# Kernel tuning notes

Hardware: AMD Instinct MI355X
Metric: run time of the kernel (lower is better)

## Reference

```python
import jax, jax.numpy as jnp
import numpy as np

B, L, C, H, NL = 128, 1024, 256, 256, 2


def setup_inputs() -> dict:
    key = jax.random.key(0)
    ks = jax.random.split(key, 10)
    s = 1.0 / np.sqrt(H)  # PyTorch GRUCell init scale
    return {
        "x": jax.random.normal(ks[0], (B, L, C), dtype=jnp.float32),
        "h0": jnp.zeros((NL, B, H), dtype=jnp.float32),
        "w_ih0": jax.random.normal(ks[1], (3 * H, C), dtype=jnp.float32) * s,
        "w_hh0": jax.random.normal(ks[2], (3 * H, H), dtype=jnp.float32) * s,
        "b_ih0": jax.random.normal(ks[3], (3 * H,), dtype=jnp.float32) * s,
        "b_hh0": jax.random.normal(ks[4], (3 * H,), dtype=jnp.float32) * s,
        "w_ih1": jax.random.normal(ks[5], (3 * H, H), dtype=jnp.float32) * s,
        "w_hh1": jax.random.normal(ks[6], (3 * H, H), dtype=jnp.float32) * s,
        "b_ih1": jax.random.normal(ks[7], (3 * H,), dtype=jnp.float32) * s,
        "b_hh1": jax.random.normal(ks[8], (3 * H,), dtype=jnp.float32) * s,
    }


def gru_cell(x, h, w_ih, w_hh, b_ih, b_hh):
    # PyTorch GRUCell math
    gi = x @ w_ih.T + b_ih          # [B, 3H]
    gh = h @ w_hh.T + b_hh          # [B, 3H]
    i_r, i_z, i_n = jnp.split(gi, 3, axis=-1)
    h_r, h_z, h_n = jnp.split(gh, 3, axis=-1)
    r = jax.nn.sigmoid(i_r + h_r)
    z = jax.nn.sigmoid(i_z + h_z)
    n = jnp.tanh(i_n + r * h_n)
    return (1.0 - z) * n + z * h


def reference(x, h0, w_ih0, w_hh0, b_ih0, b_hh0, w_ih1, w_hh1, b_ih1, b_hh1):
    # Dropout layers act as identity in eval mode (faithful deterministic reference).
    def step(carry, xt):
        h_0, h_1 = carry
        h_0 = gru_cell(xt, h_0, w_ih0, w_hh0, b_ih0, b_hh0)
        h_1 = gru_cell(h_0, h_1, w_ih1, w_hh1, b_ih1, b_hh1)
        return (h_0, h_1), h_1

    xs = jnp.swapaxes(x, 0, 1)  # [L, B, C]
    (hf0, hf1), ys = jax.lax.scan(step, (h0[0], h0[1]), xs)
    out = jnp.swapaxes(ys, 0, 1)  # [B, L, H]
    return out, jnp.stack([hf0, hf1], axis=0)
```

## Files before the change

kernel.cpp:

```cpp
#include <hip/hip_runtime.h>
#include <stdint.h>

#define Bsz 128
#define Lsz 1024
#define Hsz 256
#define HB  (Bsz * Hsz)

typedef __attribute__((ext_vector_type(8))) short bf16x8;
typedef __attribute__((ext_vector_type(4))) float f32x4;

__device__ __forceinline__ unsigned short f2bf(float f) {
    union { float f; uint32_t u; } v; v.f = f;
    uint32_t u = v.u;
    return (unsigned short)((u + 0x7FFFu + ((u >> 16) & 1u)) >> 16);
}

__device__ __forceinline__ bf16x8 load_wfrag(const float* __restrict__ W, int row, int kb) {
    const float4* p = (const float4*)(W + row * Hsz + kb);
    float4 a = p[0], b = p[1];
    bf16x8 r;
    r[0] = (short)f2bf(a.x); r[1] = (short)f2bf(a.y);
    r[2] = (short)f2bf(a.z); r[3] = (short)f2bf(a.w);
    r[4] = (short)f2bf(b.x); r[5] = (short)f2bf(b.y);
    r[6] = (short)f2bf(b.z); r[7] = (short)f2bf(b.w);
    return r;
}

__device__ __forceinline__ float sigm(float x) { return 1.0f / (1.0f + __expf(-x)); }
__device__ __forceinline__ float tanhf_(float x) { return 1.0f - 2.0f / (1.0f + __expf(2.0f * x)); }

__device__ __forceinline__ void mm_step(bf16x8 a, const bf16x8 (&W)[3][8], int kt,
                                        f32x4& r, f32x4& z, f32x4& n) {
    r = __builtin_amdgcn_mfma_f32_16x16x32_bf16(a, W[0][kt], r, 0, 0, 0);
    z = __builtin_amdgcn_mfma_f32_16x16x32_bf16(a, W[1][kt], z, 0, 0, 0);
    n = __builtin_amdgcn_mfma_f32_16x16x32_bf16(a, W[2][kt], n, 0, 0, 0);
}


__device__ __forceinline__ bf16x8 ld_h_sc1(const unsigned short* p) {
    bf16x8 r;
    asm volatile("global_load_dwordx4 %0, %1, off sc1" : "=v"(r) : "v"(p));
    return r;
}

__device__ __forceinline__ void st_h_sc1(unsigned short* p, unsigned short v) {
    unsigned int d = v;
    asm volatile("global_store_short %0, %1, off sc1" :: "v"(p), "v"(d) : "memory");
}

__device__ __forceinline__ void drain_stores_then_flag8(int* flg_base, int entry, int val, int ln) {
    asm volatile("s_waitcnt vmcnt(0)" ::: "memory");
    if (ln < 8)
        __hip_atomic_store(flg_base + (ln << 5) + entry, val,
                           __ATOMIC_RELAXED, __HIP_MEMORY_SCOPE_AGENT);
}

__device__ __forceinline__ void waitflags16(const int* f, int target, int ln) {
    const int idx = ln & 15;
    while (__hip_atomic_load(f + idx, __ATOMIC_RELAXED, __HIP_MEMORY_SCOPE_AGENT) < target) {
        __builtin_amdgcn_s_sleep(1);
    }
    asm volatile("" ::: "memory");
}

__global__ void init_ws(const float* __restrict__ h0in, int* flags,
                        unsigned short* h0buf, unsigned short* h1buf) {
    int i = blockIdx.x * blockDim.x + threadIdx.x;
    if (i < 4096)
        __hip_atomic_store(flags + i, 0, __ATOMIC_RELAXED, __HIP_MEMORY_SCOPE_AGENT);
    st_h_sc1(&h0buf[HB + i], f2bf(h0in[i]));
    st_h_sc1(&h1buf[HB + i], f2bf(h0in[HB + i]));
    asm volatile("s_waitcnt vmcnt(0)" ::: "memory");
}

__global__ __launch_bounds__(512, 2) void gru2_persist(
    const float* __restrict__ x, const float* __restrict__ h0in,
    const float* __restrict__ wih0, const float* __restrict__ whh0,
    const float* __restrict__ bih0, const float* __restrict__ bhh0,
    const float* __restrict__ wih1, const float* __restrict__ whh1,
    const float* __restrict__ bih1, const float* __restrict__ bhh1,
    float* __restrict__ out,
    int* flags0, unsigned short* h0buf, unsigned short* h1buf)
{
    __shared__ float lds0[3][2][16][16];
    __shared__ float lds1[3][2][16][16];

    const int tid = threadIdx.x;
    const int wv = tid >> 6, ln = tid & 63;
    const int lr = ln & 15, quad = ln >> 4;
    const int g = blockIdx.x & 7, p = blockIdx.x >> 3;
    const int mat = wv & 3, jt = wv >> 2;
    const int b0 = g << 4;
    const int jabs = (p << 5) + (jt << 4) + lr;

    int* fl0g = flags0 + (g << 8);
    int* fl1g = flags0 + 2048 + (g << 8);
    int* myf0 = fl0g + (p << 5);
    int* myf1 = fl1g + (p << 5);

    const float* Wm = (mat == 0) ? wih0 : (mat == 1) ? whh0 : (mat == 2) ? wih1 : whh1;
    bf16x8 Wf[3][8];
#pragma unroll
    for (int gg = 0; gg < 3; ++gg)
#pragma unroll
        for (int kt = 0; kt < 8; ++kt)
            Wf[gg][kt] = load_wfrag(Wm, gg * Hsz + jabs, (kt << 5) + (quad << 3));

    float hp[4] = {0.f, 0.f, 0.f, 0.f};
    float bsr = 0.f, bsz_ = 0.f, bin_ = 0.f, bhn_ = 0.f;
    if (mat == 1) {
#pragma unroll
        for (int q = 0; q < 4; ++q) hp[q] = h0in[(b0 + (quad << 2) + q) * Hsz + jabs];
        bsr = bih0[jabs] + bhh0[jabs];
        bsz_ = bih0[Hsz + jabs] + bhh0[Hsz + jabs];
        bin_ = bih0[2 * Hsz + jabs];
        bhn_ = bhh0[2 * Hsz + jabs];
    } else if (mat == 3) {
#pragma unroll
        for (int q = 0; q < 4; ++q) hp[q] = h0in[HB + (b0 + (quad << 2) + q) * Hsz + jabs];
        bsr = bih1[jabs] + bhh1[jabs];
        bsz_ = bih1[Hsz + jabs] + bhh1[Hsz + jabs];
        bin_ = bih1[2 * Hsz + jabs];
        bhn_ = bhh1[2 * Hsz + jabs];
    }

    const float* xrow = x + (size_t)(b0 + lr) * Lsz * Hsz;
    float4 xpre[16];
    if (mat == 0) {
#pragma unroll
        for (int kt = 0; kt < 8; ++kt) {
            const float* s = xrow + (kt << 5) + (quad << 3);
            xpre[2 * kt] = *(const float4*)(s);
            xpre[2 * kt + 1] = *(const float4*)(s + 4);
        }
    }

#pragma unroll 1
    for (int i = 0; i <= Lsz; ++i) {
        const unsigned short* h0r = h0buf + ((i ^ 1) & 1) * HB;
        unsigned short* h0w = h0buf + (i & 1) * HB;
        const unsigned short* h1r = h1buf + (i & 1) * HB;
        unsigned short* h1w = h1buf + ((i ^ 1) & 1) * HB;

        f32x4 ar = {0.f, 0.f, 0.f, 0.f}, az = {0.f, 0.f, 0.f, 0.f}, an = {0.f, 0.f, 0.f, 0.f};

        if (mat == 0) {
            if (i < Lsz) {
#pragma unroll
                for (int kt = 0; kt < 8; ++kt) {
                    float4 u = xpre[2 * kt], v = xpre[2 * kt + 1];
                    bf16x8 a;
                    a[0] = (short)f2bf(u.x); a[1] = (short)f2bf(u.y);
                    a[2] = (short)f2bf(u.z); a[3] = (short)f2bf(u.w);
                    a[4] = (short)f2bf(v.x); a[5] = (short)f2bf(v.y);
                    a[6] = (short)f2bf(v.z); a[7] = (short)f2bf(v.w);
                    mm_step(a, Wf, kt, ar, az, an);
                }
#pragma unroll
                for (int q = 0; q < 4; ++q) {
                    lds0[0][jt][(quad << 2) + q][lr] = ar[q];
                    lds0[1][jt][(quad << 2) + q][lr] = az[q];
                    lds0[2][jt][(quad << 2) + q][lr] = an[q];
                }
            }
        } else if (mat == 1) {
            if (i < Lsz) {
                waitflags16(myf0, i, ln);
                bf16x8 av[8];
#pragma unroll
                for (int kt = 0; kt < 8; ++kt)
                    av[kt] = ld_h_sc1(h0r + (b0 + lr) * Hsz + (kt << 5) + (quad << 3));
                asm volatile("s_waitcnt vmcnt(0)" ::: "memory");
                __builtin_amdgcn_sched_barrier(0);
#pragma unroll
                for (int kt = 0; kt < 8; ++kt)
                    mm_step(av[kt], Wf, kt, ar, az, an);
            }
        } else if (mat == 2) {
            if (i) {
                waitflags16(myf0, i, ln);
                bf16x8 av[8];
#pragma unroll
                for (int kt = 0; kt < 8; ++kt)
                    av[kt] = ld_h_sc1(h0r + (b0 + lr) * Hsz + (kt << 5) + (quad << 3));
                asm volatile("s_waitcnt vmcnt(0)" ::: "memory");
                __builtin_amdgcn_sched_barrier(0);
#pragma unroll
                for (int kt = 0; kt < 8; ++kt)
                    mm_step(av[kt], Wf, kt, ar, az, an);
#pragma unroll
                for (int q = 0; q < 4; ++q) {
                    lds1[0][jt][(quad << 2) + q][lr] = ar[q];
                    lds1[1][jt][(quad << 2) + q][lr] = az[q];
                    lds1[2][jt][(quad << 2) + q][lr] = an[q];
                }
            }
        } else {
            if (i) {
                waitflags16(myf1, i - 1, ln);
                bf16x8 av[8];
#pragma unroll
                for (int kt = 0; kt < 8; ++kt)
                    av[kt] = ld_h_sc1(h1r + (b0 + lr) * Hsz + (kt << 5) + (quad << 3));
                asm volatile("s_waitcnt vmcnt(0)" ::: "memory");
                __builtin_amdgcn_sched_barrier(0);
#pragma unroll
                for (int kt = 0; kt < 8; ++kt)
                    mm_step(av[kt], Wf, kt, ar, az, an);
            }
        }
        __syncthreads();

        if (mat == 1) {
            if (i < Lsz) {
#pragma unroll
                for (int q = 0; q < 4; ++q) {
                    float gir = lds0[0][jt][(quad << 2) + q][lr];
                    float giz = lds0[1][jt][(quad << 2) + q][lr];
                    float gin = lds0[2][jt][(quad << 2) + q][lr];
                    float r = sigm(gir + ar[q] + bsr);
                    float z = sigm(giz + az[q] + bsz_);
                    float n = tanhf_(gin + bin_ + r * (an[q] + bhn_));
                    float h = (1.0f - z) * n + z * hp[q];
                    hp[q] = h;
                    st_h_sc1(&h0w[(b0 + (quad << 2) + q) * Hsz + jabs], f2bf(h));
                }
                drain_stores_then_flag8(fl0g, (p << 1) + jt, i + 1, ln);
            }
        } else if (mat == 3) {
            if (i) {
                float hv[4];
#pragma unroll
                for (int q = 0; q < 4; ++q) {
                    float gir = lds1[0][jt][(quad << 2) + q][lr];
                    float giz = lds1[1][jt][(quad << 2) + q][lr];
                    float gin = lds1[2][jt][(quad << 2) + q][lr];
                    float r = sigm(gir + ar[q] + bsr);
                    float z = sigm(giz + az[q] + bsz_);
                    float n = tanhf_(gin + bin_ + r * (an[q] + bhn_));
                    float h = (1.0f - z) * n + z * hp[q];
                    hp[q] = h;
                    hv[q] = h;
                    st_h_sc1(&h1w[(b0 + (quad << 2) + q) * Hsz + jabs], f2bf(h));
                }
                drain_stores_then_flag8(fl1g, (p << 1) + jt, i, ln);
                const int t = i - 1;
#pragma unroll
                for (int q = 0; q < 4; ++q)
                    out[((size_t)(b0 + (quad << 2) + q) * Lsz + t) * Hsz + jabs] = hv[q];
            }
        } else if (mat == 0) {
            if (i + 1 < Lsz) {
                const float* xb = xrow + (size_t)(i + 1) * Hsz;
#pragma unroll
                for (int kt = 0; kt < 8; ++kt) {
                    const float* s = xb + (kt << 5) + (quad << 3);
                    xpre[2 * kt] = *(const float4*)(s);
                    xpre[2 * kt + 1] = *(const float4*)(s + 4);
                }
            }
        }
        __syncthreads();
    }

    float* hN = out + (size_t)Bsz * Lsz * Hsz;
    if (mat == 1) {
#pragma unroll
        for (int q = 0; q < 4; ++q)
            hN[(b0 + (quad << 2) + q) * Hsz + jabs] = hp[q];
    } else if (mat == 3) {
#pragma unroll
        for (int q = 0; q < 4; ++q)
            hN[HB + (b0 + (quad << 2) + q) * Hsz + jabs] = hp[q];
    }
}

extern "C" void kernel_launch(void* const* d_in, const int* in_sizes, int n_in,
                              void* d_out, int out_size, void* d_ws, size_t ws_size,
                              hipStream_t stream) {
    const float* xx   = (const float*)d_in[0];
    const float* h0   = (const float*)d_in[1];
    const float* wih0 = (const float*)d_in[2];
    const float* whh0 = (const float*)d_in[3];
    const float* bih0 = (const float*)d_in[4];
    const float* bhh0 = (const float*)d_in[5];
    const float* wih1 = (const float*)d_in[6];
    const float* whh1 = (const float*)d_in[7];
    const float* bih1 = (const float*)d_in[8];
    const float* bhh1 = (const float*)d_in[9];
    float* out = (float*)d_out;

    int* flags = (int*)d_ws;
    unsigned short* h0buf = (unsigned short*)((char*)d_ws + 16384);
    unsigned short* h1buf = h0buf + 2 * HB;

    init_ws<<<dim3(128), dim3(256), 0, stream>>>(h0, flags, h0buf, h1buf);
    gru2_persist<<<dim3(64), dim3(512), 0, stream>>>(xx, h0, wih0, whh0, bih0, bhh0,
                                                     wih1, whh1, bih1, bhh1, out,
                                                     flags, h0buf, h1buf);
}
```

Measured before the change: 4.554 ms.

## Replace flag-based cross-block sync with epoch/step-tagged hidden-state words

```diff
diff --git a/kernel.cpp b/kernel.cpp
--- a/kernel.cpp
+++ b/kernel.cpp
@@ -8,6 +8,7 @@
 
 typedef __attribute__((ext_vector_type(8))) short bf16x8;
 typedef __attribute__((ext_vector_type(4))) float f32x4;
+typedef __attribute__((ext_vector_type(4))) unsigned int u32x4;
 
 __device__ __forceinline__ unsigned short f2bf(float f) {
     union { float f; uint32_t u; } v; v.f = f;
@@ -37,39 +38,61 @@
 }
 
 
-__device__ __forceinline__ bf16x8 ld_h_sc1(const unsigned short* p) {
-    bf16x8 r;
+__device__ __forceinline__ u32x4 ld4_sc1(const uint32_t* p) {
+    u32x4 r;
     asm volatile("global_load_dwordx4 %0, %1, off sc1" : "=v"(r) : "v"(p));
     return r;
 }
 
-__device__ __forceinline__ void st_h_sc1(unsigned short* p, unsigned short v) {
-    unsigned int d = v;
-    asm volatile("global_store_short %0, %1, off sc1" :: "v"(p), "v"(d) : "memory");
-}
-
-__device__ __forceinline__ void drain_stores_then_flag8(int* flg_base, int entry, int val, int ln) {
-    asm volatile("s_waitcnt vmcnt(0)" ::: "memory");
-    if (ln < 8)
-        __hip_atomic_store(flg_base + (ln << 5) + entry, val,
-                           __ATOMIC_RELAXED, __HIP_MEMORY_SCOPE_AGENT);
-}
-
-__device__ __forceinline__ void waitflags16(const int* f, int target, int ln) {
-    const int idx = ln & 15;
-    while (__hip_atomic_load(f + idx, __ATOMIC_RELAXED, __HIP_MEMORY_SCOPE_AGENT) < target) {
-        __builtin_amdgcn_s_sleep(1);
-    }
-    asm volatile("" ::: "memory");
-}
-
-__global__ void init_ws(const float* __restrict__ h0in, int* flags,
-                        unsigned short* h0buf, unsigned short* h1buf) {
+__device__ __forceinline__ void st_dw_sc1(uint32_t* p, uint32_t d) {
+    asm volatile("global_store_dword %0, %1, off sc1" :: "v"(p), "v"(d) : "memory");
+}
+
+__device__ __forceinline__ bf16x8 pack_frag(u32x4 w0, u32x4 w1) {
+    union { uint32_t d[4]; bf16x8 v; } u;
+    u.d[0] = (w0[0] & 0xFFFFu) | (w0[1] << 16);
+    u.d[1] = (w0[2] & 0xFFFFu) | (w0[3] << 16);
+    u.d[2] = (w1[0] & 0xFFFFu) | (w1[1] << 16);
+    u.d[3] = (w1[2] & 0xFFFFu) | (w1[3] << 16);
+    return u.v;
+}
+
+__device__ __forceinline__ void poll_hrow(const uint32_t* rp, int quad,
+                                          uint32_t expect_hi, bf16x8 (&a)[8]) {
+    u32x4 w[16];
+    for (;;) {
+#pragma unroll
+        for (int kt = 0; kt < 8; ++kt) {
+            const uint32_t* s = rp + (kt << 5) + (quad << 3);
+            w[2 * kt]     = ld4_sc1(s);
+            w[2 * kt + 1] = ld4_sc1(s + 4);
+        }
+        asm volatile("s_waitcnt vmcnt(0)" ::: "memory");
+        __builtin_amdgcn_sched_barrier(0);
+        uint32_t acc = 0;
+#pragma unroll
+        for (int j = 0; j < 16; ++j)
+            acc |= (w[j][0] ^ expect_hi) | (w[j][1] ^ expect_hi)
+                 | (w[j][2] ^ expect_hi) | (w[j][3] ^ expect_hi);
+        if (__all((acc & 0xFFFF0000u) == 0u)) break;
+        __builtin_amdgcn_s_sleep(2);
+    }
+#pragma unroll
+    for (int kt = 0; kt < 8; ++kt)
+        a[kt] = pack_frag(w[2 * kt], w[2 * kt + 1]);
+}
+
+__global__ void epoch_bump(int* e) {
+    __hip_atomic_fetch_add(e, 1, __ATOMIC_RELAXED, __HIP_MEMORY_SCOPE_AGENT);
+}
+
+__global__ void init_ws(const float* __restrict__ h0in, int* epoch,
+                        uint32_t* h0buf, uint32_t* h1buf) {
     int i = blockIdx.x * blockDim.x + threadIdx.x;
-    if (i < 4096)
-        __hip_atomic_store(flags + i, 0, __ATOMIC_RELAXED, __HIP_MEMORY_SCOPE_AGENT);
-    st_h_sc1(&h0buf[HB + i], f2bf(h0in[i]));
-    st_h_sc1(&h1buf[HB + i], f2bf(h0in[HB + i]));
+    int E = __hip_atomic_load(epoch, __ATOMIC_RELAXED, __HIP_MEMORY_SCOPE_AGENT) & 31;
+    uint32_t tag_hi = ((uint32_t)(E << 11)) << 16;
+    st_dw_sc1(&h0buf[HB + i], tag_hi | f2bf(h0in[i]));
+    st_dw_sc1(&h1buf[HB + i], tag_hi | f2bf(h0in[HB + i]));
     asm volatile("s_waitcnt vmcnt(0)" ::: "memory");
 }
 
@@ -80,10 +103,10 @@
     const float* __restrict__ wih1, const float* __restrict__ whh1,
     const float* __restrict__ bih1, const float* __restrict__ bhh1,
     float* __restrict__ out,
-    int* flags0, unsigned short* h0buf, unsigned short* h1buf)
+    int* epoch, uint32_t* h0buf, uint32_t* h1buf)
 {
-    __shared__ float lds0[3][2][16][16];
-    __shared__ float lds1[3][2][16][16];
+    __shared__ float lds0[2][3][2][16][16];
+    __shared__ float lds1[2][3][2][16][16];
 
     const int tid = threadIdx.x;
     const int wv = tid >> 6, ln = tid & 63;
@@ -93,10 +116,8 @@
     const int b0 = g << 4;
     const int jabs = (p << 5) + (jt << 4) + lr;
 
-    int* fl0g = flags0 + (g << 8);
-    int* fl1g = flags0 + 2048 + (g << 8);
-    int* myf0 = fl0g + (p << 5);
-    int* myf1 = fl1g + (p << 5);
+    const uint32_t etag =
+        ((uint32_t)(__hip_atomic_load(epoch, __ATOMIC_RELAXED, __HIP_MEMORY_SCOPE_AGENT) & 31)) << 11;
 
     const float* Wm = (mat == 0) ? wih0 : (mat == 1) ? whh0 : (mat == 2) ? wih1 : whh1;
     bf16x8 Wf[3][8];
@@ -137,10 +158,11 @@
 
 #pragma unroll 1
     for (int i = 0; i <= Lsz; ++i) {
-        const unsigned short* h0r = h0buf + ((i ^ 1) & 1) * HB;
-        unsigned short* h0w = h0buf + (i & 1) * HB;
-        const unsigned short* h1r = h1buf + (i & 1) * HB;
-        unsigned short* h1w = h1buf + ((i ^ 1) & 1) * HB;
+        const int lp = i & 1;
+        const uint32_t* h0r = h0buf + ((i ^ 1) & 1) * HB;
+        uint32_t* h0w = h0buf + (i & 1) * HB;
+        const uint32_t* h1r = h1buf + (i & 1) * HB;
+        uint32_t* h1w = h1buf + ((i ^ 1) & 1) * HB;
 
         f32x4 ar = {0.f, 0.f, 0.f, 0.f}, az = {0.f, 0.f, 0.f, 0.f}, an = {0.f, 0.f, 0.f, 0.f};
 
@@ -158,52 +180,37 @@
                 }
 #pragma unroll
                 for (int q = 0; q < 4; ++q) {
-                    lds0[0][jt][(quad << 2) + q][lr] = ar[q];
-                    lds0[1][jt][(quad << 2) + q][lr] = az[q];
-                    lds0[2][jt][(quad << 2) + q][lr] = an[q];
+                    lds0[lp][0][jt][(quad << 2) + q][lr] = ar[q];
+                    lds0[lp][1][jt][(quad << 2) + q][lr] = az[q];
+                    lds0[lp][2][jt][(quad << 2) + q][lr] = an[q];
                 }
             }
         } else if (mat == 1) {
             if (i < Lsz) {
-                waitflags16(myf0, i, ln);
                 bf16x8 av[8];
-#pragma unroll
-                for (int kt = 0; kt < 8; ++kt)
-                    av[kt] = ld_h_sc1(h0r + (b0 + lr) * Hsz + (kt << 5) + (quad << 3));
-                asm volatile("s_waitcnt vmcnt(0)" ::: "memory");
-                __builtin_amdgcn_sched_barrier(0);
+                poll_hrow(h0r + (b0 + lr) * Hsz, quad, (etag | (uint32_t)i) << 16, av);
 #pragma unroll
                 for (int kt = 0; kt < 8; ++kt)
                     mm_step(av[kt], Wf, kt, ar, az, an);
             }
         } else if (mat == 2) {
             if (i) {
-                waitflags16(myf0, i, ln);
                 bf16x8 av[8];
-#pragma unroll
-                for (int kt = 0; kt < 8; ++kt)
-                    av[kt] = ld_h_sc1(h0r + (b0 + lr) * Hsz + (kt << 5) + (quad << 3));
-                asm volatile("s_waitcnt vmcnt(0)" ::: "memory");
-                __builtin_amdgcn_sched_barrier(0);
+                poll_hrow(h0r + (b0 + lr) * Hsz, quad, (etag | (uint32_t)i) << 16, av);
 #pragma unroll
                 for (int kt = 0; kt < 8; ++kt)
                     mm_step(av[kt], Wf, kt, ar, az, an);
 #pragma unroll
                 for (int q = 0; q < 4; ++q) {
-                    lds1[0][jt][(quad << 2) + q][lr] = ar[q];
-                    lds1[1][jt][(quad << 2) + q][lr] = az[q];
-                    lds1[2][jt][(quad << 2) + q][lr] = an[q];
+                    lds1[lp][0][jt][(quad << 2) + q][lr] = ar[q];
+                    lds1[lp][1][jt][(quad << 2) + q][lr] = az[q];
+                    lds1[lp][2][jt][(quad << 2) + q][lr] = an[q];
                 }
             }
         } else {
             if (i) {
-                waitflags16(myf1, i - 1, ln);
                 bf16x8 av[8];
-#pragma unroll
-                for (int kt = 0; kt < 8; ++kt)
-                    av[kt] = ld_h_sc1(h1r + (b0 + lr) * Hsz + (kt << 5) + (quad << 3));
-                asm volatile("s_waitcnt vmcnt(0)" ::: "memory");
-                __builtin_amdgcn_sched_barrier(0);
+                poll_hrow(h1r + (b0 + lr) * Hsz, quad, (etag | (uint32_t)(i - 1)) << 16, av);
 #pragma unroll
                 for (int kt = 0; kt < 8; ++kt)
                     mm_step(av[kt], Wf, kt, ar, az, an);
@@ -213,37 +220,37 @@
 
         if (mat == 1) {
             if (i < Lsz) {
+                const uint32_t wt = (etag | (uint32_t)(i + 1)) << 16;
 #pragma unroll
                 for (int q = 0; q < 4; ++q) {
-                    float gir = lds0[0][jt][(quad << 2) + q][lr];
-                    float giz = lds0[1][jt][(quad << 2) + q][lr];
-                    float gin = lds0[2][jt][(quad << 2) + q][lr];
+                    float gir = lds0[lp][0][jt][(quad << 2) + q][lr];
+                    float giz = lds0[lp][1][jt][(quad << 2) + q][lr];
+                    float gin = lds0[lp][2][jt][(quad << 2) + q][lr];
                     float r = sigm(gir + ar[q] + bsr);
                     float z = sigm(giz + az[q] + bsz_);
                     float n = tanhf_(gin + bin_ + r * (an[q] + bhn_));
                     float h = (1.0f - z) * n + z * hp[q];
                     hp[q] = h;
-                    st_h_sc1(&h0w[(b0 + (quad << 2) + q) * Hsz + jabs], f2bf(h));
-                }
-                drain_stores_then_flag8(fl0g, (p << 1) + jt, i + 1, ln);
+                    st_dw_sc1(&h0w[(b0 + (quad << 2) + q) * Hsz + jabs], wt | f2bf(h));
+                }
             }
         } else if (mat == 3) {
             if (i) {
+                const uint32_t wt = (etag | (uint32_t)i) << 16;
                 float hv[4];
 #pragma unroll
                 for (int q = 0; q < 4; ++q) {
-                    float gir = lds1[0][jt][(quad << 2) + q][lr];
-                    float giz = lds1[1][jt][(quad << 2) + q][lr];
-                    float gin = lds1[2][jt][(quad << 2) + q][lr];
+                    float gir = lds1[lp][0][jt][(quad << 2) + q][lr];
+                    float giz = lds1[lp][1][jt][(quad << 2) + q][lr];
+                    float gin = lds1[lp][2][jt][(quad << 2) + q][lr];
                     float r = sigm(gir + ar[q] + bsr);
                     float z = sigm(giz + az[q] + bsz_);
                     float n = tanhf_(gin + bin_ + r * (an[q] + bhn_));
                     float h = (1.0f - z) * n + z * hp[q];
                     hp[q] = h;
                     hv[q] = h;
-                    st_h_sc1(&h1w[(b0 + (quad << 2) + q) * Hsz + jabs], f2bf(h));
-                }
-                drain_stores_then_flag8(fl1g, (p << 1) + jt, i, ln);
+                    st_dw_sc1(&h1w[(b0 + (quad << 2) + q) * Hsz + jabs], wt | f2bf(h));
+                }
                 const int t = i - 1;
 #pragma unroll
                 for (int q = 0; q < 4; ++q)
@@ -260,7 +267,6 @@
                 }
             }
         }
-        __syncthreads();
     }
 
     float* hN = out + (size_t)Bsz * Lsz * Hsz;
@@ -290,12 +296,13 @@
     const float* bhh1 = (const float*)d_in[9];
     float* out = (float*)d_out;
 
-    int* flags = (int*)d_ws;
-    unsigned short* h0buf = (unsigned short*)((char*)d_ws + 16384);
-    unsigned short* h1buf = h0buf + 2 * HB;
-
-    init_ws<<<dim3(128), dim3(256), 0, stream>>>(h0, flags, h0buf, h1buf);
+    int* epoch = (int*)d_ws;
+    uint32_t* h0buf = (uint32_t*)((char*)d_ws + 4096);
+    uint32_t* h1buf = h0buf + 2 * HB;
+
+    epoch_bump<<<dim3(1), dim3(1), 0, stream>>>(epoch);
+    init_ws<<<dim3(128), dim3(256), 0, stream>>>(h0, epoch, h0buf, h1buf);
     gru2_persist<<<dim3(64), dim3(512), 0, stream>>>(xx, h0, wih0, whh0, bih0, bhh0,
                                                      wih1, whh1, bih1, bhh1, out,
-                                                     flags, h0buf, h1buf);
-}
+                                                     epoch, h0buf, h1buf);
+}
```

Measured after the change: 11.46 ms. 2.52x slower.
